# Kernel optimization log

Hardware: AMD Instinct MI355X
Metric: run time of the kernel (lower is better)

Reference implementation:

```python
import jax, jax.numpy as jnp
import numpy as np

B, L, E = 2, 2048, 1024
H, DKV = 16, 64


def setup_inputs() -> dict:
    key = jax.random.key(0)
    k1, k2 = jax.random.split(key)
    X = jax.random.normal(k1, (B, L, E), dtype=jnp.float32)
    # nn.Linear(embed_dim, n_heads*3*d_kv): weight stored here as [in, out]
    W_qkv = jax.random.normal(k2, (E, 3 * H * DKV), dtype=jnp.float32) * (1.0 / np.sqrt(E))
    b_qkv = jnp.zeros((3 * H * DKV,), dtype=jnp.float32)
    return {"X": X, "W_qkv": W_qkv, "b_qkv": b_qkv}


def reference(X, W_qkv, b_qkv):
    b, l, _ = X.shape
    # fused QKV projection, then 'b l (h 3*dkv)' -> [b, l, h, 3*dkv] -> chunk(3)
    qkv = (X @ W_qkv + b_qkv).reshape(b, l, H, 3 * DKV)
    Q, K, V = jnp.split(qkv, 3, axis=-1)  # each [b, l, h, dkv]
    # attn_scores: einsum('bkhd, blhd -> bhkl') / sqrt(d_kv)
    scores = jnp.einsum('bkhd,blhd->bhkl', Q, K) / np.sqrt(DKV).astype(np.float32)
    # attn_mask defaults to None -> no causal masking applied
    attn_weights = jax.nn.softmax(scores, axis=-1)  # [b, h, l, l]
    return attn_weights
```

## Files before the change

kernel.cpp:

```cpp
#include <hip/hip_runtime.h>
#include <hip/hip_bf16.h>

typedef _Float16 half4v __attribute__((ext_vector_type(4)));
typedef _Float16 half8v __attribute__((ext_vector_type(8)));
typedef float float4v __attribute__((ext_vector_type(4)));
typedef float float16v __attribute__((ext_vector_type(16)));

#define L_SEQ 2048
#define EMB 1024
#define NH 16
#define DKV 64

__device__ inline void gll16(const void* g, void* l) {
  __builtin_amdgcn_global_load_lds((const __attribute__((address_space(1))) void*)g,
                                   (__attribute__((address_space(3))) void*)l, 16, 0, 0);
}

__global__ __launch_bounds__(256) void xcast_kernel(const float* __restrict__ X,
                                                    _Float16* __restrict__ X16) {
  size_t i = ((size_t)blockIdx.x * 256 + threadIdx.x) * 8;
  float4v v0 = *(const float4v*)(X + i);
  float4v v1 = *(const float4v*)(X + i + 4);
  half8v h;
  h[0] = (_Float16)v0[0]; h[1] = (_Float16)v0[1]; h[2] = (_Float16)v0[2]; h[3] = (_Float16)v0[3];
  h[4] = (_Float16)v1[0]; h[5] = (_Float16)v1[1]; h[6] = (_Float16)v1[2]; h[7] = (_Float16)v1[3];
  *(half8v*)(X16 + i) = h;
}

__global__ __launch_bounds__(256) void wpack_kernel(const float* __restrict__ W,
                                                    _Float16* __restrict__ Wt) {
  __shared__ float tile[32][33];
  int n0 = blockIdx.x * 32;
  int k0 = blockIdx.y * 32;
  int h = n0 >> 7;
  int wc = h * 192 + (n0 & 127);
  int tx = threadIdx.x & 31;
  int ty = threadIdx.x >> 5;
#pragma unroll
  for (int i = 0; i < 4; ++i) {
    int k = ty + i * 8;
    tile[k][tx] = W[(size_t)(k0 + k) * 3072 + wc + tx];
  }
  __syncthreads();
#pragma unroll
  for (int i = 0; i < 4; ++i) {
    int n = ty + i * 8;
    Wt[(size_t)(n0 + n) * 1024 + k0 + tx] = (_Float16)tile[tx][n];
  }
}

__global__ __launch_bounds__(256, 4) void qk_gemm_kernel(const _Float16* __restrict__ X16,
                                                         const _Float16* __restrict__ Wt,
                                                         const float* __restrict__ bias,
                                                         _Float16* __restrict__ Qh,
                                                         _Float16* __restrict__ Kh) {
  __shared__ _Float16 As[128 * 64];
  __shared__ _Float16 Bs[64 * 64];
  int id = blockIdx.x;
  int xcd = id & 7;
  int rest = id >> 3;
  int n0 = (xcd * 4 + (rest & 3)) * 64;
  int m0 = (rest >> 2) * 128;
  int t = threadIdx.x;
  int l = t & 63;
  int wv = t >> 6;
  int wm = wv >> 1, wn = wv & 1;
  int cl = l & 15, hi = l >> 4;
  float4v acc[4][2] = {};
  for (int k0 = 0; k0 < 1024; k0 += 64) {
#pragma unroll
    for (int c = 0; c < 4; ++c) {
      int gi = (wv * 4 + c) * 64 + l;
      int r_ = gi >> 3, s_ = gi & 7;
      gll16(X16 + (size_t)(m0 + r_) * 1024 + k0 + 8 * (s_ ^ (r_ & 7)), &As[(wv * 4 + c) * 512]);
    }
#pragma unroll
    for (int c = 0; c < 2; ++c) {
      int gi = (wv * 2 + c) * 64 + l;
      int r_ = gi >> 3, s_ = gi & 7;
      gll16(Wt + (size_t)(n0 + r_) * 1024 + k0 + 8 * (s_ ^ (r_ & 7)), &Bs[(wv * 2 + c) * 512]);
    }
    __syncthreads();
#pragma unroll
    for (int kh = 0; kh < 2; ++kh) {
      int g = kh * 4 + hi;
      half8v a[4], b[2];
#pragma unroll
      for (int mt = 0; mt < 4; ++mt) {
        int row = wm * 64 + mt * 16 + cl;
        a[mt] = *(const half8v*)(&As[row * 64 + 8 * (g ^ (row & 7))]);
      }
#pragma unroll
      for (int nt = 0; nt < 2; ++nt) {
        int row = wn * 32 + nt * 16 + cl;
        b[nt] = *(const half8v*)(&Bs[row * 64 + 8 * (g ^ (row & 7))]);
      }
#pragma unroll
      for (int mt = 0; mt < 4; ++mt)
#pragma unroll
        for (int nt = 0; nt < 2; ++nt)
          acc[mt][nt] = __builtin_amdgcn_mfma_f32_16x16x32_f16(a[mt], b[nt], acc[mt][nt], 0, 0, 0);
    }
    __syncthreads();
  }
#pragma unroll
  for (int mt = 0; mt < 4; ++mt) {
#pragma unroll
    for (int nt = 0; nt < 2; ++nt) {
      int n_g = n0 + wn * 32 + nt * 16 + cl;
      int hh = n_g >> 7, rr = n_g & 127;
      float bv = bias[hh * 192 + rr];
      _Float16* dstbase = (rr < 64) ? Qh : Kh;
      int d = rr & 63;
#pragma unroll
      for (int r = 0; r < 4; ++r) {
        int row_g = m0 + wm * 64 + mt * 16 + hi * 4 + r;
        int bb = row_g >> 11, lr = row_g & 2047;
        dstbase[(((size_t)bb * NH + hh) * L_SEQ + lr) * DKV + d] = (_Float16)(acc[mt][nt][r] + bv);
      }
    }
  }
}

__global__ __launch_bounds__(256, 4) void attn_softmax_kernel(const _Float16* __restrict__ Qh,
                                                              const _Float16* __restrict__ Kh,
                                                              float* __restrict__ out) {
  __shared__ _Float16 Ks[2][128 * 64];
  __shared__ float sums[4][32];
  int id = blockIdx.x;
  int xcd = id & 7;
  int rest = id >> 3;
  int rb = rest & 31;
  int bh = ((rest >> 5) << 3) + xcd;
  int t = threadIdx.x;
  int l = t & 63;
  int wv = t >> 6;
  int lj = l & 31;
  int hk = l >> 5;
  int qh = wv & 1;
  int jh = wv >> 1;
  int qbase = rb * 64;
  const _Float16* Qb = Qh + ((size_t)bh * L_SEQ + qbase) * DKV;
  const _Float16* Kb = Kh + (size_t)bh * L_SEQ * DKV;
  const float SC = 0.18033688011112042f;

  half8v bq[4];
#pragma unroll
  for (int ks = 0; ks < 4; ++ks)
    bq[ks] = *(const half8v*)(Qb + (size_t)(qh * 32 + lj) * DKV + ks * 16 + hk * 8);

#define STAGE(bufi, j0)                                                     \
  {                                                                         \
    _Pragma("unroll") for (int c = 0; c < 4; ++c) {                         \
      int gi = (wv * 4 + c) * 64 + l;                                       \
      int r_ = gi >> 3, s_ = gi & 7;                                        \
      gll16(Kb + (size_t)((j0) + r_) * DKV + 8 * (s_ ^ (r_ & 7)),           \
            &Ks[bufi][(wv * 4 + c) * 512]);                                 \
    }                                                                       \
  }

  float lsum = 0.f;
  int buf = 0;
  STAGE(0, 0);
  __syncthreads();
  for (int s = 0; s < 16; ++s) {
    if (s + 1 < 16) STAGE(buf ^ 1, (s + 1) * 128);
#pragma unroll
    for (int q2 = 0; q2 < 2; ++q2) {
      int jq = jh * 2 + q2;
      int krow = jq * 32 + lj;
      half8v bk[4];
#pragma unroll
      for (int ks = 0; ks < 4; ++ks)
        bk[ks] = *(const half8v*)(&Ks[buf][krow * 64 + 8 * ((2 * ks + hk) ^ (krow & 7))]);
      float16v acc = {};
#pragma unroll
      for (int ks = 0; ks < 4; ++ks)
        acc = __builtin_amdgcn_mfma_f32_32x32x16_f16(bk[ks], bq[ks], acc, 0, 0, 0);
#pragma unroll
      for (int i = 0; i < 16; ++i) lsum += __builtin_amdgcn_exp2f(acc[i] * SC);
    }
    __syncthreads();
    buf ^= 1;
  }
  lsum += __shfl_xor(lsum, 32);
  if (l < 32) sums[wv][lj] = lsum;
  __syncthreads();

  float cc[16];
#pragma unroll
  for (int i = 0; i < 16; ++i) {
    int qo = (i & 3) + 8 * (i >> 2) + 4 * hk;
    cc[i] = -__log2f(sums[qh][qo] + sums[qh + 2][qo]);
  }

  size_t orow0 = ((size_t)bh * L_SEQ + qbase + qh * 32) * L_SEQ;
  STAGE(0, 0);
  __syncthreads();
  buf = 0;
  for (int s = 0; s < 16; ++s) {
    if (s + 1 < 16) STAGE(buf ^ 1, (s + 1) * 128);
#pragma unroll
    for (int q2 = 0; q2 < 2; ++q2) {
      int jq = jh * 2 + q2;
      int krow = jq * 32 + lj;
      half8v bk[4];
#pragma unroll
      for (int ks = 0; ks < 4; ++ks)
        bk[ks] = *(const half8v*)(&Ks[buf][krow * 64 + 8 * ((2 * ks + hk) ^ (krow & 7))]);
      float16v acc = {};
#pragma unroll
      for (int ks = 0; ks < 4; ++ks)
        acc = __builtin_amdgcn_mfma_f32_32x32x16_f16(bq[ks], bk[ks], acc, 0, 0, 0);
      size_t col = (size_t)s * 128 + jq * 32 + lj;
#pragma unroll
      for (int i = 0; i < 16; ++i) {
        float p = __builtin_amdgcn_exp2f(acc[i] * SC + cc[i]);
        int qo = (i & 3) + 8 * (i >> 2) + 4 * hk;
        __builtin_nontemporal_store(p, out + orow0 + (size_t)qo * L_SEQ + col);
      }
    }
    __syncthreads();
    buf ^= 1;
  }
#undef STAGE
}

extern "C" void kernel_launch(void* const* d_in, const int* in_sizes, int n_in,
                              void* d_out, int out_size, void* d_ws, size_t ws_size,
                              hipStream_t stream) {
  const float* X = (const float*)d_in[0];
  const float* W = (const float*)d_in[1];
  const float* bias = (const float*)d_in[2];
  float* out = (float*)d_out;
  char* ws = (char*)d_ws;
  _Float16* Wt = (_Float16*)ws;
  _Float16* Qh = (_Float16*)(ws + (4ull << 20));
  _Float16* Kh = (_Float16*)(ws + (12ull << 20));
  _Float16* X16 = (_Float16*)(ws + (20ull << 20));

  xcast_kernel<<<2048, 256, 0, stream>>>(X, X16);
  wpack_kernel<<<dim3(64, 32), 256, 0, stream>>>(W, Wt);
  qk_gemm_kernel<<<1024, 256, 0, stream>>>(X16, Wt, bias, Qh, Kh);
  attn_softmax_kernel<<<1024, 256, 0, stream>>>(Qh, Kh, out);
}
```

Measured before the change: 160.4 us.

## Load K directly into registers and overlap second half's row-sum with first half's writes

Drops the LDS double-buffered K staging and its per-iteration barriers. Each wave now loads its own 32 K rows straight from global memory into registers, prefetching two tiles ahead. The 64 query rows are split into two 32-row halves. The row-sum pass for the second half is fused into the output-write pass of the first half, so one of the two score recomputations overlaps with the store stream. This adds register pressure (launch bound lowered to 3 waves per SIMD) and relies on L2 to serve repeated K reads across waves.

```diff
diff --git a/kernel.cpp b/kernel.cpp
--- a/kernel.cpp
+++ b/kernel.cpp
@@ -122,11 +122,11 @@
   }
 }
 
-__global__ __launch_bounds__(256, 4) void attn_softmax_kernel(const _Float16* __restrict__ Qh,
+__global__ __launch_bounds__(256, 3) void attn_softmax_kernel(const _Float16* __restrict__ Qh,
                                                               const _Float16* __restrict__ Kh,
                                                               float* __restrict__ out) {
-  __shared__ _Float16 Ks[2][128 * 64];
-  __shared__ float sums[4][32];
+  __shared__ float red[4][32];
+  __shared__ float ccs[2][32];
   int id = blockIdx.x;
   int xcd = id & 7;
   int rest = id >> 3;
@@ -137,93 +137,102 @@
   int wv = t >> 6;
   int lj = l & 31;
   int hk = l >> 5;
-  int qh = wv & 1;
-  int jh = wv >> 1;
-  int qbase = rb * 64;
-  const _Float16* Qb = Qh + ((size_t)bh * L_SEQ + qbase) * DKV;
-  const _Float16* Kb = Kh + (size_t)bh * L_SEQ * DKV;
   const float SC = 0.18033688011112042f;
-
-  half8v bq[4];
-#pragma unroll
-  for (int ks = 0; ks < 4; ++ks)
-    bq[ks] = *(const half8v*)(Qb + (size_t)(qh * 32 + lj) * DKV + ks * 16 + hk * 8);
-
-#define STAGE(bufi, j0)                                                     \
-  {                                                                         \
-    _Pragma("unroll") for (int c = 0; c < 4; ++c) {                         \
-      int gi = (wv * 4 + c) * 64 + l;                                       \
-      int r_ = gi >> 3, s_ = gi & 7;                                        \
-      gll16(Kb + (size_t)((j0) + r_) * DKV + 8 * (s_ ^ (r_ & 7)),           \
-            &Ks[bufi][(wv * 4 + c) * 512]);                                 \
-    }                                                                       \
-  }
+  const _Float16* Qb = Qh + ((size_t)bh * L_SEQ + rb * 64) * DKV;
+  const _Float16* Kl = Kh + (size_t)bh * L_SEQ * DKV + (size_t)(wv * 32 + lj) * DKV + hk * 8;
+
+  half8v qa[4], qb[4];
+#pragma unroll
+  for (int ks = 0; ks < 4; ++ks) {
+    qa[ks] = *(const half8v*)(Qb + (size_t)lj * DKV + ks * 16 + hk * 8);
+    qb[ks] = *(const half8v*)(Qb + (size_t)(32 + lj) * DKV + ks * 16 + hk * 8);
+  }
+
+#define KLOAD(dst, s)                                                        \
+  _Pragma("unroll") for (int ks = 0; ks < 4; ++ks)                           \
+      dst[ks] = *(const half8v*)(Kl + (size_t)(s) * 8192 + ks * 16);
+#define ROT()                                                                \
+  _Pragma("unroll") for (int ks = 0; ks < 4; ++ks) {                         \
+    k0[ks] = k1[ks]; k1[ks] = k2[ks];                                        \
+  }
+
+  half8v k0[4], k1[4], k2[4];
 
   float lsum = 0.f;
-  int buf = 0;
-  STAGE(0, 0);
-  __syncthreads();
+  KLOAD(k0, 0);
+  KLOAD(k1, 1);
+#pragma unroll 2
   for (int s = 0; s < 16; ++s) {
-    if (s + 1 < 16) STAGE(buf ^ 1, (s + 1) * 128);
-#pragma unroll
-    for (int q2 = 0; q2 < 2; ++q2) {
-      int jq = jh * 2 + q2;
-      int krow = jq * 32 + lj;
-      half8v bk[4];
-#pragma unroll
-      for (int ks = 0; ks < 4; ++ks)
-        bk[ks] = *(const half8v*)(&Ks[buf][krow * 64 + 8 * ((2 * ks + hk) ^ (krow & 7))]);
-      float16v acc = {};
-#pragma unroll
-      for (int ks = 0; ks < 4; ++ks)
-        acc = __builtin_amdgcn_mfma_f32_32x32x16_f16(bk[ks], bq[ks], acc, 0, 0, 0);
-#pragma unroll
-      for (int i = 0; i < 16; ++i) lsum += __builtin_amdgcn_exp2f(acc[i] * SC);
-    }
-    __syncthreads();
-    buf ^= 1;
+    if (s + 2 < 16) KLOAD(k2, s + 2);
+    float16v acc = {};
+#pragma unroll
+    for (int ks = 0; ks < 4; ++ks)
+      acc = __builtin_amdgcn_mfma_f32_32x32x16_f16(k0[ks], qa[ks], acc, 0, 0, 0);
+#pragma unroll
+    for (int i = 0; i < 16; ++i) lsum += __builtin_amdgcn_exp2f(acc[i] * SC);
+    ROT();
   }
   lsum += __shfl_xor(lsum, 32);
-  if (l < 32) sums[wv][lj] = lsum;
-  __syncthreads();
-
-  float cc[16];
-#pragma unroll
-  for (int i = 0; i < 16; ++i) {
-    int qo = (i & 3) + 8 * (i >> 2) + 4 * hk;
-    cc[i] = -__log2f(sums[qh][qo] + sums[qh + 2][qo]);
-  }
-
-  size_t orow0 = ((size_t)bh * L_SEQ + qbase + qh * 32) * L_SEQ;
-  STAGE(0, 0);
-  __syncthreads();
-  buf = 0;
+  if (l < 32) red[wv][lj] = lsum;
+  __syncthreads();
+  if (t < 32) ccs[0][t] = -__log2f(red[0][t] + red[1][t] + red[2][t] + red[3][t]);
+  __syncthreads();
+  float ccA[16];
+#pragma unroll
+  for (int i = 0; i < 16; ++i) ccA[i] = ccs[0][(i & 3) + 8 * (i >> 2) + 4 * hk];
+
+  float* outA = out + ((size_t)bh * L_SEQ + rb * 64 + 4 * hk) * L_SEQ + wv * 32 + lj;
+  float lsumB = 0.f;
+  KLOAD(k0, 0);
+  KLOAD(k1, 1);
+#pragma unroll 2
   for (int s = 0; s < 16; ++s) {
-    if (s + 1 < 16) STAGE(buf ^ 1, (s + 1) * 128);
-#pragma unroll
-    for (int q2 = 0; q2 < 2; ++q2) {
-      int jq = jh * 2 + q2;
-      int krow = jq * 32 + lj;
-      half8v bk[4];
-#pragma unroll
-      for (int ks = 0; ks < 4; ++ks)
-        bk[ks] = *(const half8v*)(&Ks[buf][krow * 64 + 8 * ((2 * ks + hk) ^ (krow & 7))]);
-      float16v acc = {};
-#pragma unroll
-      for (int ks = 0; ks < 4; ++ks)
-        acc = __builtin_amdgcn_mfma_f32_32x32x16_f16(bq[ks], bk[ks], acc, 0, 0, 0);
-      size_t col = (size_t)s * 128 + jq * 32 + lj;
-#pragma unroll
-      for (int i = 0; i < 16; ++i) {
-        float p = __builtin_amdgcn_exp2f(acc[i] * SC + cc[i]);
-        int qo = (i & 3) + 8 * (i >> 2) + 4 * hk;
-        __builtin_nontemporal_store(p, out + orow0 + (size_t)qo * L_SEQ + col);
-      }
-    }
-    __syncthreads();
-    buf ^= 1;
-  }
-#undef STAGE
+    if (s + 2 < 16) KLOAD(k2, s + 2);
+    float16v accS = {};
+#pragma unroll
+    for (int ks = 0; ks < 4; ++ks)
+      accS = __builtin_amdgcn_mfma_f32_32x32x16_f16(qa[ks], k0[ks], accS, 0, 0, 0);
+#pragma unroll
+    for (int i = 0; i < 16; ++i) {
+      float p = __builtin_amdgcn_exp2f(accS[i] * SC + ccA[i]);
+      __builtin_nontemporal_store(p, outA + (size_t)((i & 3) + 8 * (i >> 2)) * L_SEQ + s * 128);
+    }
+    float16v accB = {};
+#pragma unroll
+    for (int ks = 0; ks < 4; ++ks)
+      accB = __builtin_amdgcn_mfma_f32_32x32x16_f16(k0[ks], qb[ks], accB, 0, 0, 0);
+#pragma unroll
+    for (int i = 0; i < 16; ++i) lsumB += __builtin_amdgcn_exp2f(accB[i] * SC);
+    ROT();
+  }
+  lsumB += __shfl_xor(lsumB, 32);
+  if (l < 32) red[wv][lj] = lsumB;
+  __syncthreads();
+  if (t < 32) ccs[1][t] = -__log2f(red[0][t] + red[1][t] + red[2][t] + red[3][t]);
+  __syncthreads();
+  float ccB[16];
+#pragma unroll
+  for (int i = 0; i < 16; ++i) ccB[i] = ccs[1][(i & 3) + 8 * (i >> 2) + 4 * hk];
+
+  float* outB = outA + (size_t)32 * L_SEQ;
+  KLOAD(k0, 0);
+  KLOAD(k1, 1);
+#pragma unroll 2
+  for (int s = 0; s < 16; ++s) {
+    if (s + 2 < 16) KLOAD(k2, s + 2);
+    float16v accS = {};
+#pragma unroll
+    for (int ks = 0; ks < 4; ++ks)
+      accS = __builtin_amdgcn_mfma_f32_32x32x16_f16(qb[ks], k0[ks], accS, 0, 0, 0);
+#pragma unroll
+    for (int i = 0; i < 16; ++i) {
+      float p = __builtin_amdgcn_exp2f(accS[i] * SC + ccB[i]);
+      __builtin_nontemporal_store(p, outB + (size_t)((i & 3) + 8 * (i >> 2)) * L_SEQ + s * 128);
+    }
+    ROT();
+  }
+#undef KLOAD
+#undef ROT
 }
 
 extern "C" void kernel_launch(void* const* d_in, const int* in_sizes, int n_in,
```

Result: slower. 168.7 us (+5.2%).
